# Kernel optimization log

Hardware: AMD Instinct MI355X
Metric: run time of the kernel (lower is better)

The kernel has to match this reference:

```python
import jax, jax.numpy as jnp
import numpy as np

GRID = 100  # voxel index range per axis (coors drawn in [0, GRID))
N_POINTS = 1_000_000
N_FEAT = 64
MAX_VOXELS = N_POINTS  # static upper bound on number of unique voxels


def setup_inputs() -> dict:
    key = jax.random.key(0)
    kf, kc = jax.random.split(key)
    feats = jax.random.normal(kf, (N_POINTS, N_FEAT), dtype=jnp.float32)
    coors = jax.random.randint(kc, (N_POINTS, 3), 0, GRID, dtype=jnp.int32)
    return {"feats": feats, "coors": coors}


def reference(feats, coors):
    """Dynamic point-to-voxel scatter with 'mean' reduce (average_points=True).

    Returns (voxel_feats [M_max, C], voxel_coors [M_max, 3]).
    Unique-voxel rows are packed first (sorted by linear key); padded rows
    (beyond the true voxel count M) have zero features and coors == -1.
    """
    n = feats.shape[0]
    # linear hash of 3D voxel coordinate
    keys = (coors[:, 0].astype(jnp.int64) * GRID * GRID
            + coors[:, 1].astype(jnp.int64) * GRID
            + coors[:, 2].astype(jnp.int64))
    uniq, inv = jnp.unique(keys, size=MAX_VOXELS, fill_value=-1,
                           return_inverse=True)
    inv = inv.reshape(n)
    # per-voxel sum and count -> mean
    sums = jax.ops.segment_sum(feats, inv, num_segments=MAX_VOXELS)
    counts = jax.ops.segment_sum(jnp.ones((n,), dtype=feats.dtype), inv,
                                 num_segments=MAX_VOXELS)
    voxel_feats = sums / jnp.maximum(counts, 1.0)[:, None]
    # decode unique linear keys back to 3D voxel coordinates (-1 for padding)
    valid = uniq >= 0
    u = jnp.where(valid, uniq, 0)
    cx = (u // (GRID * GRID)).astype(jnp.int32)
    cy = ((u // GRID) % GRID).astype(jnp.int32)
    cz = (u % GRID).astype(jnp.int32)
    voxel_coors = jnp.stack([cx, cy, cz], axis=-1)
    voxel_coors = jnp.where(valid[:, None], voxel_coors, -1)
    voxel_feats = jnp.where(valid[:, None], voxel_feats, 0.0)
    return voxel_feats, voxel_coors
```

## Files before the change

kernel.cpp:

```cpp
#include <hip/hip_runtime.h>

#define NPTS   1000000
#define NFEAT  64
#define GRIDN  100
#define NBINS  1000000

#define SCAN_B    256
#define SCAN_I    4
#define SCAN_TILE 1024
#define NBLK      977

__global__ void k_count(const int* __restrict__ coors, int* __restrict__ keys,
                        int* __restrict__ count, int n) {
    int p = blockIdx.x * blockDim.x + threadIdx.x;
    if (p >= n) return;
    int c0 = coors[p * 3 + 0];
    int c1 = coors[p * 3 + 1];
    int c2 = coors[p * 3 + 2];
    int key = (c0 * GRIDN + c1) * GRIDN + c2;
    keys[p] = key;
    atomicAdd(&count[key], 1);
}

__global__ void k_scan1(const int* __restrict__ count, int* __restrict__ rank,
                        int* __restrict__ pstart, int* __restrict__ blkOcc,
                        int* __restrict__ blkCnt) {
    __shared__ int sOcc[SCAN_B], sCnt[SCAN_B];
    int tid  = threadIdx.x;
    int base = blockIdx.x * SCAN_TILE + tid * SCAN_I;
    int locO[SCAN_I], locC[SCAN_I];
    int tOcc = 0, tCnt = 0;
    #pragma unroll
    for (int i = 0; i < SCAN_I; ++i) {
        int idx = base + i;
        int v = (idx < NBINS) ? count[idx] : 0;
        locO[i] = tOcc; locC[i] = tCnt;
        tOcc += (v > 0) ? 1 : 0;
        tCnt += v;
    }
    sOcc[tid] = tOcc; sCnt[tid] = tCnt;
    __syncthreads();
    for (int ofs = 1; ofs < SCAN_B; ofs <<= 1) {
        int vo = 0, vc = 0;
        if (tid >= ofs) { vo = sOcc[tid - ofs]; vc = sCnt[tid - ofs]; }
        __syncthreads();
        sOcc[tid] += vo; sCnt[tid] += vc;
        __syncthreads();
    }
    int exO = sOcc[tid] - tOcc;
    int exC = sCnt[tid] - tCnt;
    #pragma unroll
    for (int i = 0; i < SCAN_I; ++i) {
        int idx = base + i;
        if (idx < NBINS) {
            rank[idx]   = exO + locO[i];
            pstart[idx] = exC + locC[i];
        }
    }
    if (tid == SCAN_B - 1) {
        blkOcc[blockIdx.x] = sOcc[tid];
        blkCnt[blockIdx.x] = sCnt[tid];
    }
}

__global__ void k_scan2(int* __restrict__ blkOcc, int* __restrict__ blkCnt,
                        int* __restrict__ m_dev) {
    __shared__ int sO[1024], sC[1024];
    int tid = threadIdx.x;
    int vO = (tid < NBLK) ? blkOcc[tid] : 0;
    int vC = (tid < NBLK) ? blkCnt[tid] : 0;
    sO[tid] = vO; sC[tid] = vC;
    __syncthreads();
    for (int ofs = 1; ofs < 1024; ofs <<= 1) {
        int a = 0, b = 0;
        if (tid >= ofs) { a = sO[tid - ofs]; b = sC[tid - ofs]; }
        __syncthreads();
        sO[tid] += a; sC[tid] += b;
        __syncthreads();
    }
    if (tid < NBLK) {
        blkOcc[tid] = sO[tid] - vO;
        blkCnt[tid] = sC[tid] - vC;
    }
    if (tid == 1023) *m_dev = sO[1023];
}

__global__ void k_scan3(const int* __restrict__ rank, int* __restrict__ pstart,
                        const int* __restrict__ blkOcc, const int* __restrict__ blkCnt,
                        const int* __restrict__ count, int2* __restrict__ rowinfo) {
    int i = blockIdx.x * blockDim.x + threadIdx.x;
    if (i >= NBINS) return;
    int b  = i >> 10;
    int ps = pstart[i] + blkCnt[b];
    pstart[i] = ps;
    int c = count[i];
    if (c > 0) {
        int r = rank[i] + blkOcc[b];
        rowinfo[r] = make_int2(ps, i | (c << 20));
    }
}

__global__ void k_fill(const int* __restrict__ keys, int* __restrict__ pstart,
                       int* __restrict__ perm, int n) {
    int p = blockIdx.x * blockDim.x + threadIdx.x;
    if (p >= n) return;
    int pos = atomicAdd(&pstart[keys[p]], 1);
    perm[pos] = p;
}

__global__ void k_mean(const float4* __restrict__ feats4,
                       const int2* __restrict__ rowinfo,
                       const int* __restrict__ perm,
                       const int* __restrict__ m_dev,
                       float4* __restrict__ out4) {
    int gid = blockIdx.x * blockDim.x + threadIdx.x;
    int row = gid >> 4;
    int sub = gid & 15;
    if (row >= NBINS) return;
    float* out_coors = (float*)(out4 + (size_t)NBINS * 16);
    int M = *m_dev;
    if (row < M) {
        int2 info = rowinfo[row];
        int start = info.x;
        int bin   = info.y & 0xFFFFF;
        int cnt   = info.y >> 20;
        int gbase = (threadIdx.x & 63) & ~15;
        float4 s = make_float4(0.f, 0.f, 0.f, 0.f);
        for (int b0 = 0; b0 < cnt; b0 += 16) {
            int rem = cnt - b0;
            int lim = rem < 16 ? rem : 16;
            int pv  = (sub < lim) ? perm[start + b0 + sub] : 0;
            for (int j = 0; j < lim; ++j) {
                int pj = __shfl(pv, gbase + j);
                float4 f = feats4[pj * 16 + sub];
                s.x += f.x; s.y += f.y; s.z += f.z; s.w += f.w;
            }
        }
        float inv = 1.0f / (float)cnt;
        s.x *= inv; s.y *= inv; s.z *= inv; s.w *= inv;
        out4[(size_t)row * 16 + sub] = s;
        if (sub < 3) {
            int v = (sub == 0) ? bin / (GRIDN * GRIDN)
                  : (sub == 1) ? (bin / GRIDN) % GRIDN
                  :               bin % GRIDN;
            out_coors[row * 3 + sub] = (float)v;
        }
    } else {
        out4[(size_t)row * 16 + sub] = make_float4(0.f, 0.f, 0.f, 0.f);
        if (sub < 3) out_coors[row * 3 + sub] = -1.f;
    }
}

extern "C" void kernel_launch(void* const* d_in, const int* in_sizes, int n_in,
                              void* d_out, int out_size, void* d_ws, size_t ws_size,
                              hipStream_t stream) {
    const float* feats = (const float*)d_in[0];
    const int*   coors = (const int*)d_in[1];
    float*       out   = (float*)d_out;
    int n = in_sizes[1] / 3;

    int*  keys    = (int*)d_ws;
    int*  count   = keys   + NPTS;
    int*  rank    = count  + NBINS;
    int*  pstart  = rank   + NBINS;
    int*  perm    = pstart + NBINS;
    int2* rowinfo = (int2*)(perm + NPTS);
    int*  blkOcc  = (int*)(rowinfo + NBINS);
    int*  blkCnt  = blkOcc + NBLK;
    int*  m_dev   = blkCnt + NBLK;

    hipMemsetAsync(count, 0, NBINS * sizeof(int), stream);

    int b = 256;
    k_count<<<(n + b - 1) / b, b, 0, stream>>>(coors, keys, count, n);
    k_scan1<<<NBLK, SCAN_B, 0, stream>>>(count, rank, pstart, blkOcc, blkCnt);
    k_scan2<<<1, 1024, 0, stream>>>(blkOcc, blkCnt, m_dev);
    k_scan3<<<(NBINS + b - 1) / b, b, 0, stream>>>(rank, pstart, blkOcc, blkCnt,
                                                   count, rowinfo);
    k_fill<<<(n + b - 1) / b, b, 0, stream>>>(keys, pstart, perm, n);
    k_mean<<<(NBINS * 16) / b, b, 0, stream>>>((const float4*)feats, rowinfo, perm,
                                               m_dev, (float4*)out);
}
```

Before: 593.1 us.

## Use reduce-then-scan and inline the first two point indices in rowinfo

The first scan pass now only reduces per-block totals with vectorized int4 loads. The local scan moves into the third pass, so the rank array is no longer written and re-read. The fill kernel writes the first two point indices of each voxel directly into a widened int4 rowinfo record. This lets the mean kernel skip the perm lookup and shuffle loop for voxels holding one or two points. The cost is a 16-byte rowinfo entry per voxel and an extra 8-byte rankstart gather per point in the fill kernel.

```diff
diff --git a/kernel.cpp b/kernel.cpp
--- a/kernel.cpp
+++ b/kernel.cpp
@@ -22,45 +22,24 @@
     atomicAdd(&count[key], 1);
 }
 
-__global__ void k_scan1(const int* __restrict__ count, int* __restrict__ rank,
-                        int* __restrict__ pstart, int* __restrict__ blkOcc,
+__global__ void k_scan1(const int4* __restrict__ count4, int* __restrict__ blkOcc,
                         int* __restrict__ blkCnt) {
-    __shared__ int sOcc[SCAN_B], sCnt[SCAN_B];
+    __shared__ int sO[SCAN_B], sC[SCAN_B];
     int tid  = threadIdx.x;
     int base = blockIdx.x * SCAN_TILE + tid * SCAN_I;
-    int locO[SCAN_I], locC[SCAN_I];
-    int tOcc = 0, tCnt = 0;
-    #pragma unroll
-    for (int i = 0; i < SCAN_I; ++i) {
-        int idx = base + i;
-        int v = (idx < NBINS) ? count[idx] : 0;
-        locO[i] = tOcc; locC[i] = tCnt;
-        tOcc += (v > 0) ? 1 : 0;
-        tCnt += v;
-    }
-    sOcc[tid] = tOcc; sCnt[tid] = tCnt;
+    int tO = 0, tC = 0;
+    if (base < NBINS) {
+        int4 v = count4[base >> 2];
+        tO = (v.x > 0) + (v.y > 0) + (v.z > 0) + (v.w > 0);
+        tC = v.x + v.y + v.z + v.w;
+    }
+    sO[tid] = tO; sC[tid] = tC;
     __syncthreads();
-    for (int ofs = 1; ofs < SCAN_B; ofs <<= 1) {
-        int vo = 0, vc = 0;
-        if (tid >= ofs) { vo = sOcc[tid - ofs]; vc = sCnt[tid - ofs]; }
-        __syncthreads();
-        sOcc[tid] += vo; sCnt[tid] += vc;
-        __syncthreads();
-    }
-    int exO = sOcc[tid] - tOcc;
-    int exC = sCnt[tid] - tCnt;
-    #pragma unroll
-    for (int i = 0; i < SCAN_I; ++i) {
-        int idx = base + i;
-        if (idx < NBINS) {
-            rank[idx]   = exO + locO[i];
-            pstart[idx] = exC + locC[i];
-        }
-    }
-    if (tid == SCAN_B - 1) {
-        blkOcc[blockIdx.x] = sOcc[tid];
-        blkCnt[blockIdx.x] = sCnt[tid];
-    }
+    for (int ofs = SCAN_B / 2; ofs > 0; ofs >>= 1) {
+        if (tid < ofs) { sO[tid] += sO[tid + ofs]; sC[tid] += sC[tid + ofs]; }
+        __syncthreads();
+    }
+    if (tid == 0) { blkOcc[blockIdx.x] = sO[0]; blkCnt[blockIdx.x] = sC[0]; }
 }
 
 __global__ void k_scan2(int* __restrict__ blkOcc, int* __restrict__ blkCnt,
@@ -85,31 +64,68 @@
     if (tid == 1023) *m_dev = sO[1023];
 }
 
-__global__ void k_scan3(const int* __restrict__ rank, int* __restrict__ pstart,
+__global__ void k_scan3(const int4* __restrict__ count4, int4* __restrict__ pstart4,
                         const int* __restrict__ blkOcc, const int* __restrict__ blkCnt,
-                        const int* __restrict__ count, int2* __restrict__ rowinfo) {
-    int i = blockIdx.x * blockDim.x + threadIdx.x;
-    if (i >= NBINS) return;
-    int b  = i >> 10;
-    int ps = pstart[i] + blkCnt[b];
-    pstart[i] = ps;
-    int c = count[i];
-    if (c > 0) {
-        int r = rank[i] + blkOcc[b];
-        rowinfo[r] = make_int2(ps, i | (c << 20));
+                        long long* __restrict__ rankstart, int4* __restrict__ rowinfo) {
+    __shared__ int sO[SCAN_B], sC[SCAN_B];
+    int tid  = threadIdx.x;
+    int base = blockIdx.x * SCAN_TILE + tid * SCAN_I;
+    int4 v = make_int4(0, 0, 0, 0);
+    if (base < NBINS) v = count4[base >> 2];
+    int c[SCAN_I] = {v.x, v.y, v.z, v.w};
+    int locO[SCAN_I], locC[SCAN_I];
+    int tO = 0, tC = 0;
+    #pragma unroll
+    for (int i = 0; i < SCAN_I; ++i) {
+        locO[i] = tO; locC[i] = tC;
+        tO += (c[i] > 0) ? 1 : 0;
+        tC += c[i];
+    }
+    sO[tid] = tO; sC[tid] = tC;
+    __syncthreads();
+    for (int ofs = 1; ofs < SCAN_B; ofs <<= 1) {
+        int a = 0, b = 0;
+        if (tid >= ofs) { a = sO[tid - ofs]; b = sC[tid - ofs]; }
+        __syncthreads();
+        sO[tid] += a; sC[tid] += b;
+        __syncthreads();
+    }
+    if (base >= NBINS) return;
+    int exO = sO[tid] - tO + blkOcc[blockIdx.x];
+    int exC = sC[tid] - tC + blkCnt[blockIdx.x];
+    int4 ps;
+    ps.x = exC + locC[0]; ps.y = exC + locC[1];
+    ps.z = exC + locC[2]; ps.w = exC + locC[3];
+    pstart4[base >> 2] = ps;
+    int psa[SCAN_I] = {ps.x, ps.y, ps.z, ps.w};
+    #pragma unroll
+    for (int i = 0; i < SCAN_I; ++i) {
+        if (c[i] > 0) {
+            int bin = base + i;
+            int r   = exO + locO[i];
+            rankstart[bin] = ((long long)r << 32) | (long long)psa[i];
+            *(int2*)(&rowinfo[r]) = make_int2(psa[i], bin | (c[i] << 20));
+        }
     }
 }
 
 __global__ void k_fill(const int* __restrict__ keys, int* __restrict__ pstart,
-                       int* __restrict__ perm, int n) {
+                       const long long* __restrict__ rankstart,
+                       int* __restrict__ perm, int4* __restrict__ rowinfo, int n) {
     int p = blockIdx.x * blockDim.x + threadIdx.x;
     if (p >= n) return;
-    int pos = atomicAdd(&pstart[keys[p]], 1);
-    perm[pos] = p;
+    int k = keys[p];
+    int pos = atomicAdd(&pstart[k], 1);
+    long long rs = rankstart[k];
+    int start = (int)(rs & 0xFFFFFFFFLL);
+    int r     = (int)(rs >> 32);
+    int j = pos - start;
+    if (j < 2) ((int*)rowinfo)[r * 4 + 2 + j] = p;
+    else       perm[pos] = p;
 }
 
 __global__ void k_mean(const float4* __restrict__ feats4,
-                       const int2* __restrict__ rowinfo,
+                       const int4* __restrict__ rowinfo,
                        const int* __restrict__ perm,
                        const int* __restrict__ m_dev,
                        float4* __restrict__ out4) {
@@ -120,20 +136,26 @@
     float* out_coors = (float*)(out4 + (size_t)NBINS * 16);
     int M = *m_dev;
     if (row < M) {
-        int2 info = rowinfo[row];
+        int4 info = rowinfo[row];
         int start = info.x;
         int bin   = info.y & 0xFFFFF;
         int cnt   = info.y >> 20;
-        int gbase = (threadIdx.x & 63) & ~15;
-        float4 s = make_float4(0.f, 0.f, 0.f, 0.f);
-        for (int b0 = 0; b0 < cnt; b0 += 16) {
-            int rem = cnt - b0;
-            int lim = rem < 16 ? rem : 16;
-            int pv  = (sub < lim) ? perm[start + b0 + sub] : 0;
-            for (int j = 0; j < lim; ++j) {
-                int pj = __shfl(pv, gbase + j);
-                float4 f = feats4[pj * 16 + sub];
-                s.x += f.x; s.y += f.y; s.z += f.z; s.w += f.w;
+        float4 s = feats4[(size_t)info.z * 16 + sub];
+        if (cnt > 1) {
+            float4 f = feats4[(size_t)info.w * 16 + sub];
+            s.x += f.x; s.y += f.y; s.z += f.z; s.w += f.w;
+        }
+        if (cnt > 2) {
+            int gbase = (threadIdx.x & 63) & ~15;
+            for (int b0 = 2; b0 < cnt; b0 += 16) {
+                int rem = cnt - b0;
+                int lim = rem < 16 ? rem : 16;
+                int pv  = (sub < lim) ? perm[start + b0 + sub] : 0;
+                for (int j = 0; j < lim; ++j) {
+                    int pj = __shfl(pv, gbase + j);
+                    float4 f = feats4[(size_t)pj * 16 + sub];
+                    s.x += f.x; s.y += f.y; s.z += f.z; s.w += f.w;
+                }
             }
         }
         float inv = 1.0f / (float)cnt;
@@ -159,25 +181,26 @@
     float*       out   = (float*)d_out;
     int n = in_sizes[1] / 3;
 
-    int*  keys    = (int*)d_ws;
-    int*  count   = keys   + NPTS;
-    int*  rank    = count  + NBINS;
-    int*  pstart  = rank   + NBINS;
-    int*  perm    = pstart + NBINS;
-    int2* rowinfo = (int2*)(perm + NPTS);
-    int*  blkOcc  = (int*)(rowinfo + NBINS);
-    int*  blkCnt  = blkOcc + NBLK;
-    int*  m_dev   = blkCnt + NBLK;
+    int*       keys      = (int*)d_ws;
+    int*       count     = keys   + NPTS;
+    int*       pstart    = count  + NBINS;
+    int*       perm      = pstart + NBINS;
+    int4*      rowinfo   = (int4*)(perm + NPTS);
+    long long* rankstart = (long long*)(rowinfo + NBINS);
+    int*       blkOcc    = (int*)(rankstart + NBINS);
+    int*       blkCnt    = blkOcc + NBLK;
+    int*       m_dev     = blkCnt + NBLK;
 
     hipMemsetAsync(count, 0, NBINS * sizeof(int), stream);
 
     int b = 256;
     k_count<<<(n + b - 1) / b, b, 0, stream>>>(coors, keys, count, n);
-    k_scan1<<<NBLK, SCAN_B, 0, stream>>>(count, rank, pstart, blkOcc, blkCnt);
+    k_scan1<<<NBLK, SCAN_B, 0, stream>>>((const int4*)count, blkOcc, blkCnt);
     k_scan2<<<1, 1024, 0, stream>>>(blkOcc, blkCnt, m_dev);
-    k_scan3<<<(NBINS + b - 1) / b, b, 0, stream>>>(rank, pstart, blkOcc, blkCnt,
-                                                   count, rowinfo);
-    k_fill<<<(n + b - 1) / b, b, 0, stream>>>(keys, pstart, perm, n);
+    k_scan3<<<NBLK, SCAN_B, 0, stream>>>((const int4*)count, (int4*)pstart,
+                                         blkOcc, blkCnt, rankstart, rowinfo);
+    k_fill<<<(n + b - 1) / b, b, 0, stream>>>(keys, pstart, rankstart, perm,
+                                              rowinfo, n);
     k_mean<<<(NBINS * 16) / b, b, 0, stream>>>((const float4*)feats, rowinfo, perm,
                                                m_dev, (float4*)out);
 }
```

Result: faster. 558.4 us (-5.8%).
